# Kernel tuning notes

Measured on AMD Instinct MI355X. Metric: run time of the kernel, lower is better.

Reference implementation:

```python
import jax, jax.numpy as jnp
import numpy as np

R, CH, N, E, C, OUT, ED = 2, 2, 20000, 100000, 256, 256, 16


def setup_inputs() -> dict:
    key = jax.random.key(0)
    ks = jax.random.split(key, 11)
    inv = 1.0 / np.sqrt(C)
    return {
        "x": jax.random.normal(ks[0], (R * CH * N, C), jnp.float32),
        "edge_attr": jax.random.normal(ks[1], (E, ED), jnp.float32),
        "edge_weight": jax.random.uniform(ks[2], (R, CH, E, 1), jnp.float32),
        "lin_W": jax.random.normal(ks[3], (C, C), jnp.float32) * inv,
        "lin_b": jax.random.normal(ks[4], (C,), jnp.float32) * inv,
        "linl_W": jax.random.normal(ks[5], (C, OUT), jnp.float32) * inv,
        "linl_b": jax.random.normal(ks[6], (OUT,), jnp.float32) * inv,
        "linr_W": jax.random.normal(ks[7], (C, OUT), jnp.float32) * inv,
        "bond_W": jax.random.normal(ks[8], (ED, C), jnp.float32) / np.sqrt(ED),
        "bond_b": jax.random.normal(ks[9], (C,), jnp.float32) / np.sqrt(ED),
        "edge_index": jax.random.randint(ks[10], (2, E), 0, N, jnp.int64),
    }


def reference(x, edge_attr, edge_weight, lin_W, lin_b, linl_W, linl_b, linr_W,
              bond_W, bond_b, edge_index):
    # bond encoder: (E, ED) -> (E, C), broadcasts as (1, 1, E, C)
    edge_emb = edge_attr @ bond_W + bond_b
    x_l = x @ lin_W + lin_b                      # (R*CH*N, C)
    ux = x_l.reshape(R, CH, N, C)
    src = edge_index[0]
    dst = edge_index[1]
    # gather + add + GELU (exact/erf, matching torch F.gelu) + weight
    msg = jax.nn.gelu(ux[:, :, src, :] + edge_emb, approximate=False) * edge_weight  # (R,CH,E,C)
    # scatter_mean over edge targets
    sums = jnp.zeros((R, CH, N, C), x.dtype).at[:, :, dst, :].add(msg)
    cnt = jnp.zeros((N,), x.dtype).at[dst].add(1.0)
    out = sums / jnp.maximum(cnt, 1.0)[None, None, :, None]
    out = out.reshape(-1, C)                     # (R*CH*N, C)
    return out @ linl_W + linl_b + x @ linr_W
```

## Files before the change

### kernel.cpp

```cpp
#include <hip/hip_runtime.h>
#include <math.h>

#define NN 20000
#define EE 100000
#define CC 256
#define EDM 16
#define RC 4
#define MTOT (RC * NN)

typedef __attribute__((ext_vector_type(8))) short short8;
typedef __attribute__((ext_vector_type(4))) float floatx4;

__device__ __forceinline__ unsigned short f2bf(float f) {
    union { float f; unsigned u; } v; v.f = f;
    unsigned r = v.u + 0x7FFF + ((v.u >> 16) & 1);
    return (unsigned short)(r >> 16);
}
__device__ __forceinline__ float uif(unsigned u) {
    union { unsigned u; float f; } v; v.u = u;
    return v.f;
}

__device__ __forceinline__ float gelu27(float v) {
    const float z  = fabsf(v) * 0.70710678118654752f;
    const float P  = fmaf(z, fmaf(z, fmaf(z, fmaf(z, 0.078108f, 0.000972f),
                           0.230389f), 0.278393f), 1.0f);
    const float r  = __builtin_amdgcn_rcpf(P);
    const float r2 = r * r;
    const float r4 = r2 * r2;
    const float h  = 0.5f * fabsf(v);
    return fmaf(0.5f, v, fmaf(-h, r4, h));
}

#define GLDS16(gp, lp)                                                        \
    __builtin_amdgcn_global_load_lds(                                         \
        (const __attribute__((address_space(1))) unsigned int*)(gp),          \
        (__attribute__((address_space(3))) unsigned int*)(lp), 16, 0, 0)

__global__ void k_prep_count(const float* __restrict__ lin_W,
                             const float* __restrict__ linl_W,
                             const float* __restrict__ linr_W,
                             unsigned short* __restrict__ linWT,
                             unsigned short* __restrict__ WbT,
                             const int* __restrict__ eidx,
                             int* __restrict__ cnt) {
    const int b = blockIdx.x;
    const int t = threadIdx.x;
    if (b < CC) {
        linWT[b * CC + t]      = f2bf(lin_W[t * CC + b]);
        WbT[b * 512 + t]       = f2bf(linl_W[t * CC + b]);
        WbT[b * 512 + 256 + t] = f2bf(linr_W[t * CC + b]);
    } else {
        int e = (b - CC) * 256 + t;
        if (e < EE) atomicAdd(cnt + eidx[EE + e], 1);
    }
}

__global__ __launch_bounds__(256) void k_mm1(const float* __restrict__ x,
                                             const unsigned short* __restrict__ linWT,
                                             const float* __restrict__ lin_b,
                                             unsigned short* __restrict__ xlb4,
                                             unsigned short* __restrict__ xb) {
    __shared__ unsigned short SH[2][128 * 64];
    unsigned short* As = SH[0];
    unsigned short* Bs = SH[1];
    const int tid  = threadIdx.x;
    const int lane = tid & 63;
    const int wave = tid >> 6;
    const int wr   = wave >> 1;
    const int wc   = wave & 1;
    const int l15  = lane & 15;
    const int q4   = lane >> 4;
    const int lr8  = lane >> 3;
    const int lc8  = lane & 7;
    const int nn0  = blockIdx.x * 32;
    const int n0h  = blockIdx.y * 128;
    const int emit_xb = (xb != nullptr) && (blockIdx.y == 0);

    floatx4 acc[4][4];
#pragma unroll
    for (int mt = 0; mt < 4; mt++)
#pragma unroll
        for (int nt = 0; nt < 4; nt++) acc[mt][nt] = (floatx4)0.0f;

    for (int kc = 0; kc < 256; kc += 64) {
        __syncthreads();
#pragma unroll
        for (int it = 0; it < 4; it++) {
            const int op = wave * 4 + it;
            const unsigned short* g =
                linWT + (size_t)(n0h + op * 8 + lr8) * CC + kc + lc8 * 8;
            GLDS16(g, Bs + op * 512);
        }
#pragma unroll
        for (int w = 0; w < 4; w++) {
            const int q  = w * 256 + tid;
            const int r  = q >> 3;
            const int c8 = q & 7;
            const int grow = (r >> 5) * NN + nn0 + (r & 31);
            const float* s = x + (size_t)grow * CC + kc + c8 * 8;
            float4 v0 = *(const float4*)(s);
            float4 v1 = *(const float4*)(s + 4);
            uint4 p;
            p.x = (unsigned)f2bf(v0.x) | ((unsigned)f2bf(v0.y) << 16);
            p.y = (unsigned)f2bf(v0.z) | ((unsigned)f2bf(v0.w) << 16);
            p.z = (unsigned)f2bf(v1.x) | ((unsigned)f2bf(v1.y) << 16);
            p.w = (unsigned)f2bf(v1.z) | ((unsigned)f2bf(v1.w) << 16);
            *(uint4*)(As + r * 64 + c8 * 8) = p;
            if (emit_xb)
                *(uint4*)(xb + (size_t)grow * CC + kc + c8 * 8) = p;
        }
        __syncthreads();
#pragma unroll
        for (int kk = 0; kk < 64; kk += 32) {
            short8 a[4], b[4];
#pragma unroll
            for (int mt = 0; mt < 4; mt++)
                a[mt] = *(const short8*)(As + (wr * 64 + mt * 16 + l15) * 64 + kk + q4 * 8);
#pragma unroll
            for (int nt = 0; nt < 4; nt++)
                b[nt] = *(const short8*)(Bs + (wc * 64 + nt * 16 + l15) * 64 + kk + q4 * 8);
#pragma unroll
            for (int mt = 0; mt < 4; mt++)
#pragma unroll
                for (int nt = 0; nt < 4; nt++)
                    acc[mt][nt] = __builtin_amdgcn_mfma_f32_16x16x32_bf16(
                        a[mt], b[nt], acc[mt][nt], 0, 0, 0);
        }
    }
    __syncthreads();
    char* E = (char*)SH;
#pragma unroll
    for (int nt = 0; nt < 4; nt++) {
        const int cl = wc * 64 + nt * 16 + l15;
        const float bz = lin_b[n0h + cl];
#pragma unroll
        for (int m0 = 0; m0 < 2; m0++) {
#pragma unroll
            for (int rr = 0; rr < 4; rr++) {
                const int i = m0 * 16 + q4 * 4 + rr;
                const unsigned lo = f2bf(acc[m0][nt][rr] + bz);
                const unsigned hi = f2bf(acc[m0 + 2][nt][rr] + bz);
                *(unsigned*)(E + i * 1024 + cl * 8 + wr * 4) = lo | (hi << 16);
            }
        }
    }
    __syncthreads();
    char* gbase = (char*)xlb4 + (size_t)nn0 * 2048 + (size_t)n0h * 8;
#pragma unroll
    for (int p = 0; p < 8; p++) {
        const int idx = p * 256 + tid;
        const int i   = idx >> 6;
        const int w   = (idx & 63) * 16;
        uint4 v = *(const uint4*)(E + i * 1024 + w);
        *(uint4*)(gbase + (size_t)i * 2048 + w) = v;
    }
}

template <int XB>
__global__ __launch_bounds__(256) void k_mm2(const unsigned short* __restrict__ mean_b,
                                             const unsigned short* __restrict__ xb,
                                             const float* __restrict__ xf,
                                             const unsigned short* __restrict__ WbT,
                                             const float* __restrict__ bias,
                                             float* __restrict__ out) {
    __shared__ unsigned short As[128 * 64];
    __shared__ unsigned short Bs[128 * 64];
    const int tid  = threadIdx.x;
    const int lane = tid & 63;
    const int wave = tid >> 6;
    const int wr   = wave >> 1;
    const int wc   = wave & 1;
    const int l15  = lane & 15;
    const int q4   = lane >> 4;
    const int lr8  = lane >> 3;
    const int lc8  = lane & 7;
    const int i0   = blockIdx.x * 128;
    const int n0   = blockIdx.y * 128;

    floatx4 acc[4][4];
#pragma unroll
    for (int mt = 0; mt < 4; mt++)
#pragma unroll
        for (int nt = 0; nt < 4; nt++) acc[mt][nt] = (floatx4)0.0f;

    for (int kc = 0; kc < 512; kc += 64) {
        __syncthreads();
        const int first = (kc < 256);
        const int kco   = first ? kc : kc - 256;
#pragma unroll
        for (int it = 0; it < 4; it++) {
            const int op = wave * 4 + it;
            const unsigned short* g =
                WbT + (size_t)(n0 + op * 8 + lr8) * 512 + kc + lc8 * 8;
            GLDS16(g, Bs + op * 512);
        }
        if (first || XB) {
            const unsigned short* ab = first ? mean_b : xb;
#pragma unroll
            for (int it = 0; it < 4; it++) {
                const int op = wave * 4 + it;
                const unsigned short* g =
                    ab + (size_t)(i0 + op * 8 + lr8) * CC + kco + lc8 * 8;
                GLDS16(g, As + op * 512);
            }
        } else {
#pragma unroll
            for (int w = 0; w < 4; w++) {
                const int q  = w * 256 + tid;
                const int r  = q >> 3;
                const int c8 = q & 7;
                const float* s = xf + (size_t)(i0 + r) * CC + kco + c8 * 8;
                float4 v0 = *(const float4*)(s);
                float4 v1 = *(const float4*)(s + 4);
                uint4 p;
                p.x = (unsigned)f2bf(v0.x) | ((unsigned)f2bf(v0.y) << 16);
                p.y = (unsigned)f2bf(v0.z) | ((unsigned)f2bf(v0.w) << 16);
                p.z = (unsigned)f2bf(v1.x) | ((unsigned)f2bf(v1.y) << 16);
                p.w = (unsigned)f2bf(v1.z) | ((unsigned)f2bf(v1.w) << 16);
                *(uint4*)(As + r * 64 + c8 * 8) = p;
            }
        }
        __syncthreads();
#pragma unroll
        for (int kk = 0; kk < 64; kk += 32) {
            short8 a[4], b[4];
#pragma unroll
            for (int mt = 0; mt < 4; mt++)
                a[mt] = *(const short8*)(As + (wr * 64 + mt * 16 + l15) * 64 + kk + q4 * 8);
#pragma unroll
            for (int nt = 0; nt < 4; nt++)
                b[nt] = *(const short8*)(Bs + (wc * 64 + nt * 16 + l15) * 64 + kk + q4 * 8);
#pragma unroll
            for (int mt = 0; mt < 4; mt++)
#pragma unroll
                for (int nt = 0; nt < 4; nt++)
                    acc[mt][nt] = __builtin_amdgcn_mfma_f32_16x16x32_bf16(
                        a[mt], b[nt], acc[mt][nt], 0, 0, 0);
        }
    }
#pragma unroll
    for (int nt = 0; nt < 4; nt++) {
        const int col = n0 + wc * 64 + nt * 16 + l15;
        const float bz = bias[col];
#pragma unroll
        for (int mt = 0; mt < 4; mt++) {
#pragma unroll
            for (int r = 0; r < 4; r++) {
                const int row = i0 + wr * 64 + mt * 16 + q4 * 4 + r;
                out[(size_t)row * CC + col] = acc[mt][nt][r] + bz;
            }
        }
    }
}

#define SCAN_T 1024
#define SCHUNK 20
__global__ __launch_bounds__(1024) void k_scan(const int* __restrict__ cnt,
                                               int* __restrict__ offs,
                                               int* __restrict__ cursor) {
    __shared__ int ps[SCAN_T];
    const int t = threadIdx.x;
    const int base = t * SCHUNK;
    int s = 0;
#pragma unroll
    for (int i = 0; i < SCHUNK; i++) {
        int idx = base + i;
        if (idx < NN) s += cnt[idx];
    }
    ps[t] = s;
    __syncthreads();
    for (int off = 1; off < SCAN_T; off <<= 1) {
        int v = (t >= off) ? ps[t - off] : 0;
        __syncthreads();
        ps[t] += v;
        __syncthreads();
    }
    int excl = (t == 0) ? 0 : ps[t - 1];
#pragma unroll
    for (int i = 0; i < SCHUNK; i++) {
        int idx = base + i;
        if (idx < NN) {
            offs[idx]   = excl;
            cursor[idx] = excl;
            excl += cnt[idx];
        }
    }
    if (t == SCAN_T - 1) offs[NN] = ps[SCAN_T - 1];
}

__global__ void k_scatter(const int* __restrict__ eidx,
                          const float* __restrict__ ew,
                          int* __restrict__ cursor,
                          int* __restrict__ bucket,
                          int* __restrict__ srcb,
                          float4* __restrict__ ewb) {
    int e = blockIdx.x * 256 + threadIdx.x;
    if (e < EE) {
        int d = eidx[EE + e];
        int p = atomicAdd(cursor + d, 1);
        bucket[p] = e;
        srcb[p]   = eidx[e];
        ewb[p]    = make_float4(ew[e], ew[EE + e], ew[2 * EE + e], ew[3 * EE + e]);
    }
}

__global__ __launch_bounds__(256) void k_agg(const unsigned short* __restrict__ xlb4,
                                             const float* __restrict__ edge_attr,
                                             const float4* __restrict__ ewb,
                                             const float* __restrict__ bond_W,
                                             const float* __restrict__ bond_b,
                                             const int* __restrict__ srcb,
                                             const int* __restrict__ offs,
                                             const int* __restrict__ bucket,
                                             unsigned short* __restrict__ mean_b) {
    const int n = blockIdx.x;
    const int c = threadIdx.x;
    const int beg = offs[n], end = offs[n + 1];
    const float bb = bond_b[c];
    float bw[EDM];
#pragma unroll
    for (int k = 0; k < EDM; k++) bw[k] = bond_W[k * CC + c];

    float a0 = 0.f, a1 = 0.f, a2 = 0.f, a3 = 0.f;

#pragma unroll 2
    for (int j = beg; j < end; j++) {
        const int e     = bucket[j];
        const int src   = srcb[j];
        const float4 w  = ewb[j];
        const float4* ea4 = (const float4*)(edge_attr + (size_t)e * EDM);
        const float4 q0 = ea4[0], q1 = ea4[1], q2 = ea4[2], q3 = ea4[3];
        float emb = bb;
        emb = fmaf(q0.x, bw[0],  emb); emb = fmaf(q0.y, bw[1],  emb);
        emb = fmaf(q0.z, bw[2],  emb); emb = fmaf(q0.w, bw[3],  emb);
        emb = fmaf(q1.x, bw[4],  emb); emb = fmaf(q1.y, bw[5],  emb);
        emb = fmaf(q1.z, bw[6],  emb); emb = fmaf(q1.w, bw[7],  emb);
        emb = fmaf(q2.x, bw[8],  emb); emb = fmaf(q2.y, bw[9],  emb);
        emb = fmaf(q2.z, bw[10], emb); emb = fmaf(q2.w, bw[11], emb);
        emb = fmaf(q3.x, bw[12], emb); emb = fmaf(q3.y, bw[13], emb);
        emb = fmaf(q3.z, bw[14], emb); emb = fmaf(q3.w, bw[15], emb);
        const uint2 u = *(const uint2*)(xlb4 + ((size_t)src * CC + c) * 4);
        const float v0 = uif(u.x << 16)          + emb;
        const float v1 = uif(u.x & 0xffff0000u)  + emb;
        const float v2 = uif(u.y << 16)          + emb;
        const float v3 = uif(u.y & 0xffff0000u)  + emb;
        a0 = fmaf(gelu27(v0), w.x, a0);
        a1 = fmaf(gelu27(v1), w.y, a1);
        a2 = fmaf(gelu27(v2), w.z, a2);
        a3 = fmaf(gelu27(v3), w.w, a3);
    }
    const float inv = 1.0f / fmaxf((float)(end - beg), 1.0f);
    const size_t ob = (size_t)n * CC + c;
    mean_b[ob]                       = f2bf(a0 * inv);
    mean_b[ob + (size_t)NN * CC]     = f2bf(a1 * inv);
    mean_b[ob + (size_t)2 * NN * CC] = f2bf(a2 * inv);
    mean_b[ob + (size_t)3 * NN * CC] = f2bf(a3 * inv);
}

extern "C" void kernel_launch(void* const* d_in, const int* in_sizes, int n_in,
                              void* d_out, int out_size, void* d_ws, size_t ws_size,
                              hipStream_t stream) {
    (void)in_sizes; (void)n_in; (void)out_size;
    const float* x           = (const float*)d_in[0];
    const float* edge_attr   = (const float*)d_in[1];
    const float* edge_weight = (const float*)d_in[2];
    const float* lin_W       = (const float*)d_in[3];
    const float* lin_b       = (const float*)d_in[4];
    const float* linl_W      = (const float*)d_in[5];
    const float* linl_b      = (const float*)d_in[6];
    const float* linr_W      = (const float*)d_in[7];
    const float* bond_W      = (const float*)d_in[8];
    const float* bond_b      = (const float*)d_in[9];
    const int*   edge_index  = (const int*)d_in[10];

    unsigned short* xlb4  = (unsigned short*)d_ws;
    unsigned short* linWT = xlb4 + (size_t)MTOT * CC;
    unsigned short* WbT   = linWT + CC * CC;
    int* cnt    = (int*)(WbT + CC * 512);
    int* offs   = cnt + NN;
    int* cursor = offs + NN + 1;
    int* bucket = cursor + NN;
    uintptr_t mb_addr = (((uintptr_t)(bucket + EE)) + 255) & ~(uintptr_t)255;
    unsigned short* mean_b = (unsigned short*)mb_addr;
    unsigned short* xb     = mean_b + (size_t)MTOT * CC;
    const size_t need_xb = ((uintptr_t)(xb + (size_t)MTOT * CC)) - (uintptr_t)d_ws;
    const int use_xb = (ws_size >= need_xb);

    float4* ewb  = (float4*)d_out;
    int*    srcb = (int*)(ewb + EE);

    hipMemsetAsync(cnt, 0, NN * sizeof(int), stream);

    k_prep_count<<<CC + (EE + 255) / 256, 256, 0, stream>>>(
        lin_W, linl_W, linr_W, linWT, WbT, edge_index, cnt);
    k_mm1<<<dim3(NN / 32, 2), 256, 0, stream>>>(x, linWT, lin_b, xlb4,
                                                use_xb ? xb : nullptr);
    k_scan<<<1, SCAN_T, 0, stream>>>(cnt, offs, cursor);
    k_scatter<<<(EE + 255) / 256, 256, 0, stream>>>(edge_index, edge_weight,
                                                    cursor, bucket, srcb, ewb);
    k_agg<<<NN, 256, 0, stream>>>(xlb4, edge_attr, ewb, bond_W, bond_b,
                                  srcb, offs, bucket, mean_b);
    if (use_xb)
        k_mm2<1><<<dim3(MTOT / 128, 2), 256, 0, stream>>>(
            mean_b, xb, nullptr, WbT, linl_b, (float*)d_out);
    else
        k_mm2<0><<<dim3(MTOT / 128, 2), 256, 0, stream>>>(
            mean_b, nullptr, x, WbT, linl_b, (float*)d_out);
}
```

Baseline: 356.8 us.

## Use 512-thread swizzled GEMM tiles, precast x to bf16, batch agg nodes

Both GEMM kernels move to 512 threads (8 waves, each with a 4x2 accumulator tile) and XOR-swizzle the LDS layout to avoid bank conflicts. The epilogue staging stride is padded. The fp32-to-bf16 conversion of x moves into the prep kernel, so mm1 can load bf16 tiles directly through global_load_lds. The aggregation kernel handles 8 nodes per block, which amortizes the bond_W register loads. This adds a separate pass over x to write xb, and the fewer, larger agg blocks may balance load less evenly across nodes.

```diff
diff --git a/kernel.cpp b/kernel.cpp
--- a/kernel.cpp
+++ b/kernel.cpp
@@ -7,6 +7,9 @@
 #define EDM 16
 #define RC 4
 #define MTOT (RC * NN)
+#define NPB 8
+#define PREPB ((EE + 255) / 256)
+#define CONVB 10000
 
 typedef __attribute__((ext_vector_type(8))) short short8;
 typedef __attribute__((ext_vector_type(4))) float floatx4;
@@ -37,103 +40,129 @@
         (const __attribute__((address_space(1))) unsigned int*)(gp),          \
         (__attribute__((address_space(3))) unsigned int*)(lp), 16, 0, 0)
 
-__global__ void k_prep_count(const float* __restrict__ lin_W,
-                             const float* __restrict__ linl_W,
-                             const float* __restrict__ linr_W,
-                             unsigned short* __restrict__ linWT,
-                             unsigned short* __restrict__ WbT,
-                             const int* __restrict__ eidx,
-                             int* __restrict__ cnt) {
+__global__ void k_prep(const float* __restrict__ lin_W,
+                       const float* __restrict__ linl_W,
+                       const float* __restrict__ linr_W,
+                       unsigned short* __restrict__ linWT,
+                       unsigned short* __restrict__ WbT,
+                       const int* __restrict__ eidx,
+                       int* __restrict__ cnt,
+                       const float* __restrict__ x,
+                       unsigned short* __restrict__ xb) {
     const int b = blockIdx.x;
     const int t = threadIdx.x;
     if (b < CC) {
         linWT[b * CC + t]      = f2bf(lin_W[t * CC + b]);
         WbT[b * 512 + t]       = f2bf(linl_W[t * CC + b]);
         WbT[b * 512 + 256 + t] = f2bf(linr_W[t * CC + b]);
-    } else {
+    } else if (b < CC + PREPB) {
         int e = (b - CC) * 256 + t;
         if (e < EE) atomicAdd(cnt + eidx[EE + e], 1);
-    }
-}
-
-__global__ __launch_bounds__(256) void k_mm1(const float* __restrict__ x,
-                                             const unsigned short* __restrict__ linWT,
-                                             const float* __restrict__ lin_b,
-                                             unsigned short* __restrict__ xlb4,
-                                             unsigned short* __restrict__ xb) {
-    __shared__ unsigned short SH[2][128 * 64];
-    unsigned short* As = SH[0];
-    unsigned short* Bs = SH[1];
+    } else {
+        const size_t i8 = (size_t)(b - CC - PREPB) * 2048 + t * 8;
+        const float4 v0 = *(const float4*)(x + i8);
+        const float4 v1 = *(const float4*)(x + i8 + 4);
+        uint4 p;
+        p.x = (unsigned)f2bf(v0.x) | ((unsigned)f2bf(v0.y) << 16);
+        p.y = (unsigned)f2bf(v0.z) | ((unsigned)f2bf(v0.w) << 16);
+        p.z = (unsigned)f2bf(v1.x) | ((unsigned)f2bf(v1.y) << 16);
+        p.w = (unsigned)f2bf(v1.z) | ((unsigned)f2bf(v1.w) << 16);
+        *(uint4*)(xb + i8) = p;
+    }
+}
+
+template <int XB>
+__global__ __launch_bounds__(512, 4) void k_mm1(const float* __restrict__ xf,
+                                                const unsigned short* __restrict__ xb,
+                                                const unsigned short* __restrict__ linWT,
+                                                const float* __restrict__ lin_b,
+                                                unsigned short* __restrict__ xlb4) {
+    __shared__ __attribute__((aligned(16))) char SH[33280];
+    unsigned short* As = (unsigned short*)SH;
+    unsigned short* Bs = As + 128 * 64;
     const int tid  = threadIdx.x;
     const int lane = tid & 63;
     const int wave = tid >> 6;
-    const int wr   = wave >> 1;
-    const int wc   = wave & 1;
+    const int wr   = wave >> 2;
+    const int wc   = wave & 3;
     const int l15  = lane & 15;
     const int q4   = lane >> 4;
     const int lr8  = lane >> 3;
     const int lc8  = lane & 7;
+    const int sc8  = (lc8 ^ lr8) * 8;
     const int nn0  = blockIdx.x * 32;
-    const int n0h  = blockIdx.y * 128;
-    const int emit_xb = (xb != nullptr) && (blockIdx.y == 0);
-
-    floatx4 acc[4][4];
+    const int n0   = blockIdx.y * 128;
+
+    floatx4 acc[4][2];
 #pragma unroll
     for (int mt = 0; mt < 4; mt++)
 #pragma unroll
-        for (int nt = 0; nt < 4; nt++) acc[mt][nt] = (floatx4)0.0f;
+        for (int nt = 0; nt < 2; nt++) acc[mt][nt] = (floatx4)0.0f;
 
     for (int kc = 0; kc < 256; kc += 64) {
         __syncthreads();
 #pragma unroll
-        for (int it = 0; it < 4; it++) {
-            const int op = wave * 4 + it;
-            const unsigned short* g =
-                linWT + (size_t)(n0h + op * 8 + lr8) * CC + kc + lc8 * 8;
-            GLDS16(g, Bs + op * 512);
-        }
-#pragma unroll
-        for (int w = 0; w < 4; w++) {
-            const int q  = w * 256 + tid;
-            const int r  = q >> 3;
-            const int c8 = q & 7;
-            const int grow = (r >> 5) * NN + nn0 + (r & 31);
-            const float* s = x + (size_t)grow * CC + kc + c8 * 8;
-            float4 v0 = *(const float4*)(s);
-            float4 v1 = *(const float4*)(s + 4);
-            uint4 p;
-            p.x = (unsigned)f2bf(v0.x) | ((unsigned)f2bf(v0.y) << 16);
-            p.y = (unsigned)f2bf(v0.z) | ((unsigned)f2bf(v0.w) << 16);
-            p.z = (unsigned)f2bf(v1.x) | ((unsigned)f2bf(v1.y) << 16);
-            p.w = (unsigned)f2bf(v1.z) | ((unsigned)f2bf(v1.w) << 16);
-            *(uint4*)(As + r * 64 + c8 * 8) = p;
-            if (emit_xb)
-                *(uint4*)(xb + (size_t)grow * CC + kc + c8 * 8) = p;
+        for (int it = 0; it < 2; it++) {
+            const int op = wave * 2 + it;
+            GLDS16(linWT + (size_t)(n0 + op * 8 + lr8) * CC + kc + sc8,
+                   Bs + op * 512);
+        }
+        if (XB) {
+#pragma unroll
+            for (int it = 0; it < 2; it++) {
+                const int op = wave * 2 + it;
+                const int r  = op * 8 + lr8;
+                const int grow = (r >> 5) * NN + nn0 + (r & 31);
+                GLDS16(xb + (size_t)grow * CC + kc + sc8, As + op * 512);
+            }
+        } else {
+#pragma unroll
+            for (int w = 0; w < 2; w++) {
+                const int q  = w * 512 + tid;
+                const int r  = q >> 3;
+                const int c8 = q & 7;
+                const int grow = (r >> 5) * NN + nn0 + (r & 31);
+                const float* s = xf + (size_t)grow * CC + kc + c8 * 8;
+                float4 v0 = *(const float4*)(s);
+                float4 v1 = *(const float4*)(s + 4);
+                uint4 p;
+                p.x = (unsigned)f2bf(v0.x) | ((unsigned)f2bf(v0.y) << 16);
+                p.y = (unsigned)f2bf(v0.z) | ((unsigned)f2bf(v0.w) << 16);
+                p.z = (unsigned)f2bf(v1.x) | ((unsigned)f2bf(v1.y) << 16);
+                p.w = (unsigned)f2bf(v1.z) | ((unsigned)f2bf(v1.w) << 16);
+                *(uint4*)(As + r * 64 + ((c8 ^ (r & 7)) * 8)) = p;
+            }
         }
         __syncthreads();
 #pragma unroll
         for (int kk = 0; kk < 64; kk += 32) {
-            short8 a[4], b[4];
+            short8 a[4], b[2];
+#pragma unroll
+            for (int mt = 0; mt < 4; mt++) {
+                const int row = wr * 64 + mt * 16 + l15;
+                a[mt] = *(const short8*)(As + row * 64 +
+                                         ((kk + q4 * 8) ^ ((row & 7) * 8)));
+            }
+#pragma unroll
+            for (int nt = 0; nt < 2; nt++) {
+                const int row = wc * 32 + nt * 16 + l15;
+                b[nt] = *(const short8*)(Bs + row * 64 +
+                                         ((kk + q4 * 8) ^ ((row & 7) * 8)));
+            }
 #pragma unroll
             for (int mt = 0; mt < 4; mt++)
-                a[mt] = *(const short8*)(As + (wr * 64 + mt * 16 + l15) * 64 + kk + q4 * 8);
-#pragma unroll
-            for (int nt = 0; nt < 4; nt++)
-                b[nt] = *(const short8*)(Bs + (wc * 64 + nt * 16 + l15) * 64 + kk + q4 * 8);
-#pragma unroll
-            for (int mt = 0; mt < 4; mt++)
-#pragma unroll
-                for (int nt = 0; nt < 4; nt++)
+#pragma unroll
+                for (int nt = 0; nt < 2; nt++)
                     acc[mt][nt] = __builtin_amdgcn_mfma_f32_16x16x32_bf16(
                         a[mt], b[nt], acc[mt][nt], 0, 0, 0);
         }
     }
     __syncthreads();
-    char* E = (char*)SH;
-#pragma unroll
-    for (int nt = 0; nt < 4; nt++) {
-        const int cl = wc * 64 + nt * 16 + l15;
-        const float bz = lin_b[n0h + cl];
+    char* E = SH;
+#pragma unroll
+    for (int nt = 0; nt < 2; nt++) {
+        const int cl = wc * 32 + nt * 16 + l15;
+        const float bz = lin_b[n0 + cl];
 #pragma unroll
         for (int m0 = 0; m0 < 2; m0++) {
 #pragma unroll
@@ -141,73 +170,72 @@
                 const int i = m0 * 16 + q4 * 4 + rr;
                 const unsigned lo = f2bf(acc[m0][nt][rr] + bz);
                 const unsigned hi = f2bf(acc[m0 + 2][nt][rr] + bz);
-                *(unsigned*)(E + i * 1024 + cl * 8 + wr * 4) = lo | (hi << 16);
+                *(unsigned*)(E + i * 1040 + cl * 8 + wr * 4) = lo | (hi << 16);
             }
         }
     }
     __syncthreads();
-    char* gbase = (char*)xlb4 + (size_t)nn0 * 2048 + (size_t)n0h * 8;
-#pragma unroll
-    for (int p = 0; p < 8; p++) {
-        const int idx = p * 256 + tid;
+    char* gb = (char*)xlb4 + (size_t)nn0 * 2048 + (size_t)n0 * 8;
+#pragma unroll
+    for (int p = 0; p < 4; p++) {
+        const int idx = p * 512 + tid;
         const int i   = idx >> 6;
         const int w   = (idx & 63) * 16;
-        uint4 v = *(const uint4*)(E + i * 1024 + w);
-        *(uint4*)(gbase + (size_t)i * 2048 + w) = v;
+        uint4 v = *(const uint4*)(E + i * 1040 + w);
+        *(uint4*)(gb + (size_t)i * 2048 + w) = v;
     }
 }
 
 template <int XB>
-__global__ __launch_bounds__(256) void k_mm2(const unsigned short* __restrict__ mean_b,
-                                             const unsigned short* __restrict__ xb,
-                                             const float* __restrict__ xf,
-                                             const unsigned short* __restrict__ WbT,
-                                             const float* __restrict__ bias,
-                                             float* __restrict__ out) {
+__global__ __launch_bounds__(512, 4) void k_mm2(const unsigned short* __restrict__ mean_b,
+                                                const unsigned short* __restrict__ xb,
+                                                const float* __restrict__ xf,
+                                                const unsigned short* __restrict__ WbT,
+                                                const float* __restrict__ bias,
+                                                float* __restrict__ out) {
     __shared__ unsigned short As[128 * 64];
     __shared__ unsigned short Bs[128 * 64];
     const int tid  = threadIdx.x;
     const int lane = tid & 63;
     const int wave = tid >> 6;
-    const int wr   = wave >> 1;
-    const int wc   = wave & 1;
+    const int wr   = wave >> 2;
+    const int wc   = wave & 3;
     const int l15  = lane & 15;
     const int q4   = lane >> 4;
     const int lr8  = lane >> 3;
     const int lc8  = lane & 7;
+    const int sc8  = (lc8 ^ lr8) * 8;
     const int i0   = blockIdx.x * 128;
     const int n0   = blockIdx.y * 128;
 
-    floatx4 acc[4][4];
+    floatx4 acc[4][2];
 #pragma unroll
     for (int mt = 0; mt < 4; mt++)
 #pragma unroll
-        for (int nt = 0; nt < 4; nt++) acc[mt][nt] = (floatx4)0.0f;
+        for (int nt = 0; nt < 2; nt++) acc[mt][nt] = (floatx4)0.0f;
 
     for (int kc = 0; kc < 512; kc += 64) {
         __syncthreads();
         const int first = (kc < 256);
         const int kco   = first ? kc : kc - 256;
 #pragma unroll
-        for (int it = 0; it < 4; it++) {
-            const int op = wave * 4 + it;
-            const unsigned short* g =
-                WbT + (size_t)(n0 + op * 8 + lr8) * 512 + kc + lc8 * 8;
-            GLDS16(g, Bs + op * 512);
+        for (int it = 0; it < 2; it++) {
+            const int op = wave * 2 + it;
+            GLDS16(WbT + (size_t)(n0 + op * 8 + lr8) * 512 + kc + sc8,
+                   Bs + op * 512);
         }
         if (first || XB) {
             const unsigned short* ab = first ? mean_b : xb;
 #pragma unroll
-            for (int it = 0; it < 4; it++) {
-                const int op = wave * 4 + it;
-                const unsigned short* g =
-                    ab + (size_t)(i0 + op * 8 + lr8) * CC + kco + lc8 * 8;
-                GLDS16(g, As + op * 512);
+            for (int it = 0; it < 2; it++) {
+                const int op = wave * 2 + it;
+                GLDS16(ab + (size_t)(i0 + op * 8 + lr8) * CC + kco + sc8,
+                       As + op * 512);
             }
         } else {
 #pragma unroll
-            for (int w = 0; w < 4; w++) {
-                const int q  = w * 256 + tid;
+            for (int w = 0; w < 2; w++) {
+                const int q  = w * 512 + tid;
                 const int r  = q >> 3;
                 const int c8 = q & 7;
                 const float* s = xf + (size_t)(i0 + r) * CC + kco + c8 * 8;
@@ -218,37 +246,43 @@
                 p.y = (unsigned)f2bf(v0.z) | ((unsigned)f2bf(v0.w) << 16);
                 p.z = (unsigned)f2bf(v1.x) | ((unsigned)f2bf(v1.y) << 16);
                 p.w = (unsigned)f2bf(v1.z) | ((unsigned)f2bf(v1.w) << 16);
-                *(uint4*)(As + r * 64 + c8 * 8) = p;
+                *(uint4*)(As + r * 64 + ((c8 ^ (r & 7)) * 8)) = p;
             }
         }
         __syncthreads();
 #pragma unroll
         for (int kk = 0; kk < 64; kk += 32) {
-            short8 a[4], b[4];
+            short8 a[4], b[2];
+#pragma unroll
+            for (int mt = 0; mt < 4; mt++) {
+                const int row = wr * 64 + mt * 16 + l15;
+                a[mt] = *(const short8*)(As + row * 64 +
+                                         ((kk + q4 * 8) ^ ((row & 7) * 8)));
+            }
+#pragma unroll
+            for (int nt = 0; nt < 2; nt++) {
+                const int row = wc * 32 + nt * 16 + l15;
+                b[nt] = *(const short8*)(Bs + row * 64 +
+                                         ((kk + q4 * 8) ^ ((row & 7) * 8)));
+            }
 #pragma unroll
             for (int mt = 0; mt < 4; mt++)
-                a[mt] = *(const short8*)(As + (wr * 64 + mt * 16 + l15) * 64 + kk + q4 * 8);
-#pragma unroll
-            for (int nt = 0; nt < 4; nt++)
-                b[nt] = *(const short8*)(Bs + (wc * 64 + nt * 16 + l15) * 64 + kk + q4 * 8);
-#pragma unroll
-            for (int mt = 0; mt < 4; mt++)
-#pragma unroll
-                for (int nt = 0; nt < 4; nt++)
+#pragma unroll
+                for (int nt = 0; nt < 2; nt++)
                     acc[mt][nt] = __builtin_amdgcn_mfma_f32_16x16x32_bf16(
                         a[mt], b[nt], acc[mt][nt], 0, 0, 0);
         }
     }
 #pragma unroll
-    for (int nt = 0; nt < 4; nt++) {
-        const int col = n0 + wc * 64 + nt * 16 + l15;
+    for (int nt = 0; nt < 2; nt++) {
+        const int col = n0 + wc * 32 + nt * 16 + l15;
         const float bz = bias[col];
 #pragma unroll
         for (int mt = 0; mt < 4; mt++) {
 #pragma unroll
-            for (int r = 0; r < 4; r++) {
-                const int row = i0 + wr * 64 + mt * 16 + q4 * 4 + r;
-                out[(size_t)row * CC + col] = acc[mt][nt][r] + bz;
+            for (int rr = 0; rr < 4; rr++) {
+                const int row = i0 + wr * 64 + mt * 16 + q4 * 4 + rr;
+                out[(size_t)row * CC + col] = acc[mt][nt][rr] + bz;
             }
         }
     }
@@ -314,48 +348,51 @@
                                              const int* __restrict__ offs,
                                              const int* __restrict__ bucket,
                                              unsigned short* __restrict__ mean_b) {
-    const int n = blockIdx.x;
     const int c = threadIdx.x;
-    const int beg = offs[n], end = offs[n + 1];
     const float bb = bond_b[c];
     float bw[EDM];
 #pragma unroll
     for (int k = 0; k < EDM; k++) bw[k] = bond_W[k * CC + c];
-
-    float a0 = 0.f, a1 = 0.f, a2 = 0.f, a3 = 0.f;
+    const int nbase = blockIdx.x * NPB;
+
+    for (int nn = 0; nn < NPB; nn++) {
+        const int n = nbase + nn;
+        const int beg = offs[n], end = offs[n + 1];
+        float a0 = 0.f, a1 = 0.f, a2 = 0.f, a3 = 0.f;
 
 #pragma unroll 2
-    for (int j = beg; j < end; j++) {
-        const int e     = bucket[j];
-        const int src   = srcb[j];
-        const float4 w  = ewb[j];
-        const float4* ea4 = (const float4*)(edge_attr + (size_t)e * EDM);
-        const float4 q0 = ea4[0], q1 = ea4[1], q2 = ea4[2], q3 = ea4[3];
-        float emb = bb;
-        emb = fmaf(q0.x, bw[0],  emb); emb = fmaf(q0.y, bw[1],  emb);
-        emb = fmaf(q0.z, bw[2],  emb); emb = fmaf(q0.w, bw[3],  emb);
-        emb = fmaf(q1.x, bw[4],  emb); emb = fmaf(q1.y, bw[5],  emb);
-        emb = fmaf(q1.z, bw[6],  emb); emb = fmaf(q1.w, bw[7],  emb);
-        emb = fmaf(q2.x, bw[8],  emb); emb = fmaf(q2.y, bw[9],  emb);
-        emb = fmaf(q2.z, bw[10], emb); emb = fmaf(q2.w, bw[11], emb);
-        emb = fmaf(q3.x, bw[12], emb); emb = fmaf(q3.y, bw[13], emb);
-        emb = fmaf(q3.z, bw[14], emb); emb = fmaf(q3.w, bw[15], emb);
-        const uint2 u = *(const uint2*)(xlb4 + ((size_t)src * CC + c) * 4);
-        const float v0 = uif(u.x << 16)          + emb;
-        const float v1 = uif(u.x & 0xffff0000u)  + emb;
-        const float v2 = uif(u.y << 16)          + emb;
-        const float v3 = uif(u.y & 0xffff0000u)  + emb;
-        a0 = fmaf(gelu27(v0), w.x, a0);
-        a1 = fmaf(gelu27(v1), w.y, a1);
-        a2 = fmaf(gelu27(v2), w.z, a2);
-        a3 = fmaf(gelu27(v3), w.w, a3);
-    }
-    const float inv = 1.0f / fmaxf((float)(end - beg), 1.0f);
-    const size_t ob = (size_t)n * CC + c;
-    mean_b[ob]                       = f2bf(a0 * inv);
-    mean_b[ob + (size_t)NN * CC]     = f2bf(a1 * inv);
-    mean_b[ob + (size_t)2 * NN * CC] = f2bf(a2 * inv);
-    mean_b[ob + (size_t)3 * NN * CC] = f2bf(a3 * inv);
+        for (int j = beg; j < end; j++) {
+            const int e     = bucket[j];
+            const int src   = srcb[j];
+            const float4 w  = ewb[j];
+            const float4* ea4 = (const float4*)(edge_attr + (size_t)e * EDM);
+            const float4 q0 = ea4[0], q1 = ea4[1], q2 = ea4[2], q3 = ea4[3];
+            float emb = bb;
+            emb = fmaf(q0.x, bw[0],  emb); emb = fmaf(q0.y, bw[1],  emb);
+            emb = fmaf(q0.z, bw[2],  emb); emb = fmaf(q0.w, bw[3],  emb);
+            emb = fmaf(q1.x, bw[4],  emb); emb = fmaf(q1.y, bw[5],  emb);
+            emb = fmaf(q1.z, bw[6],  emb); emb = fmaf(q1.w, bw[7],  emb);
+            emb = fmaf(q2.x, bw[8],  emb); emb = fmaf(q2.y, bw[9],  emb);
+            emb = fmaf(q2.z, bw[10], emb); emb = fmaf(q2.w, bw[11], emb);
+            emb = fmaf(q3.x, bw[12], emb); emb = fmaf(q3.y, bw[13], emb);
+            emb = fmaf(q3.z, bw[14], emb); emb = fmaf(q3.w, bw[15], emb);
+            const uint2 u = *(const uint2*)(xlb4 + ((size_t)src * CC + c) * 4);
+            const float v0 = uif(u.x << 16)          + emb;
+            const float v1 = uif(u.x & 0xffff0000u)  + emb;
+            const float v2 = uif(u.y << 16)          + emb;
+            const float v3 = uif(u.y & 0xffff0000u)  + emb;
+            a0 = fmaf(gelu27(v0), w.x, a0);
+            a1 = fmaf(gelu27(v1), w.y, a1);
+            a2 = fmaf(gelu27(v2), w.z, a2);
+            a3 = fmaf(gelu27(v3), w.w, a3);
+        }
+        const float inv = 1.0f / fmaxf((float)(end - beg), 1.0f);
+        const size_t ob = (size_t)n * CC + c;
+        mean_b[ob]                       = f2bf(a0 * inv);
+        mean_b[ob + (size_t)NN * CC]     = f2bf(a1 * inv);
+        mean_b[ob + (size_t)2 * NN * CC] = f2bf(a2 * inv);
+        mean_b[ob + (size_t)3 * NN * CC] = f2bf(a3 * inv);
+    }
 }
 
 extern "C" void kernel_launch(void* const* d_in, const int* in_sizes, int n_in,
@@ -392,19 +429,22 @@
 
     hipMemsetAsync(cnt, 0, NN * sizeof(int), stream);
 
-    k_prep_count<<<CC + (EE + 255) / 256, 256, 0, stream>>>(
-        lin_W, linl_W, linr_W, linWT, WbT, edge_index, cnt);
-    k_mm1<<<dim3(NN / 32, 2), 256, 0, stream>>>(x, linWT, lin_b, xlb4,
-                                                use_xb ? xb : nullptr);
+    k_prep<<<CC + PREPB + (use_xb ? CONVB : 0), 256, 0, stream>>>(
+        lin_W, linl_W, linr_W, linWT, WbT, edge_index, cnt, x,
+        use_xb ? xb : nullptr);
+    if (use_xb)
+        k_mm1<1><<<dim3(NN / 32, 2), 512, 0, stream>>>(nullptr, xb, linWT, lin_b, xlb4);
+    else
+        k_mm1<0><<<dim3(NN / 32, 2), 512, 0, stream>>>(x, nullptr, linWT, lin_b, xlb4);
     k_scan<<<1, SCAN_T, 0, stream>>>(cnt, offs, cursor);
-    k_scatter<<<(EE + 255) / 256, 256, 0, stream>>>(edge_index, edge_weight,
-                                                    cursor, bucket, srcb, ewb);
-    k_agg<<<NN, 256, 0, stream>>>(xlb4, edge_attr, ewb, bond_W, bond_b,
-                                  srcb, offs, bucket, mean_b);
+    k_scatter<<<PREPB, 256, 0, stream>>>(edge_index, edge_weight,
+                                         cursor, bucket, srcb, ewb);
+    k_agg<<<NN / NPB, 256, 0, stream>>>(xlb4, edge_attr, ewb, bond_W, bond_b,
+                                        srcb, offs, bucket, mean_b);
     if (use_xb)
-        k_mm2<1><<<dim3(MTOT / 128, 2), 256, 0, stream>>>(
+        k_mm2<1><<<dim3(MTOT / 128, 2), 512, 0, stream>>>(
             mean_b, xb, nullptr, WbT, linl_b, (float*)d_out);
     else
-        k_mm2<0><<<dim3(MTOT / 128, 2), 256, 0, stream>>>(
+        k_mm2<0><<<dim3(MTOT / 128, 2), 512, 0, stream>>>(
             mean_b, nullptr, x, WbT, linl_b, (float*)d_out);
 }
```

New measurement: 348.1 us. 2.4% less time.
